# Kernel optimization log

Measured on AMD Instinct MI355X. Metric: run time of the kernel, lower is better.

The kernel has to match this reference:

```python
import jax, jax.numpy as jnp
import numpy as np

NUM_QUERIES = 900
EMBED_DIM = 256
NUM_HEADS = 8
EPS = 1e-5


def bilinear_sample(feats, grid):
    """F.grid_sample(..., align_corners=False, padding_mode='zeros', bilinear).
    feats: [BN, C, H, W], grid: [BN, Q, 2] in [-1,1] (x, y). Returns [BN, Q, C]."""
    BN, C, H, W = feats.shape
    ix = (grid[..., 0] + 1.0) * (W * 0.5) - 0.5
    iy = (grid[..., 1] + 1.0) * (H * 0.5) - 0.5
    x0 = jnp.floor(ix)
    y0 = jnp.floor(iy)
    wx1 = ix - x0
    wy1 = iy - y0
    x0i = x0.astype(jnp.int32)
    y0i = y0.astype(jnp.int32)
    x1i = x0i + 1
    y1i = y0i + 1
    b = jnp.arange(BN)[:, None]

    def gather(yy, xx):
        inb = (xx >= 0) & (xx < W) & (yy >= 0) & (yy < H)
        yc = jnp.clip(yy, 0, H - 1)
        xc = jnp.clip(xx, 0, W - 1)
        v = feats[b, :, yc, xc]  # [BN, Q, C]
        return v * inb[..., None].astype(feats.dtype)

    out = (gather(y0i, x0i) * ((1 - wx1) * (1 - wy1))[..., None]
           + gather(y0i, x1i) * (wx1 * (1 - wy1))[..., None]
           + gather(y1i, x0i) * ((1 - wx1) * wy1)[..., None]
           + gather(y1i, x1i) * (wx1 * wy1)[..., None])
    return out


def setup_inputs() -> dict:
    key = jax.random.key(0)
    ks = jax.random.split(key, 16)
    B, N, C, H, W = 2, 6, 256, 116, 200
    Q, D = NUM_QUERIES, EMBED_DIM
    s = 0.02
    return {
        "image_features": jax.random.normal(ks[0], (B, N, C, H, W), jnp.float32),
        "lidar2img": jax.random.normal(ks[1], (B, N, 4, 4), jnp.float32),
        "query_embedding": jax.random.normal(ks[2], (Q, D), jnp.float32) * s,
        "ref_w": jax.random.normal(ks[3], (3, D), jnp.float32) * s,
        "ref_b": jnp.zeros((3,), jnp.float32),
        "in_proj_w": jax.random.normal(ks[4], (3 * D, D), jnp.float32) * s,
        "in_proj_b": jnp.zeros((3 * D,), jnp.float32),
        "out_proj_w": jax.random.normal(ks[5], (D, D), jnp.float32) * s,
        "out_proj_b": jnp.zeros((D,), jnp.float32),
        "norm_w": jnp.ones((D,), jnp.float32),
        "norm_b": jnp.zeros((D,), jnp.float32),
        "cls_w": jax.random.normal(ks[6], (2, D), jnp.float32) * s,
        "cls_b": jnp.zeros((2,), jnp.float32),
        "box_w": jax.random.normal(ks[7], (6, D), jnp.float32) * s,
        "box_b": jnp.zeros((6,), jnp.float32),
    }


def reference(image_features, lidar2img, query_embedding, ref_w, ref_b,
              in_proj_w, in_proj_b, out_proj_w, out_proj_b,
              norm_w, norm_b, cls_w, cls_b, box_w, box_b):
    B, N, C, H, W = image_features.shape
    Q, D = query_embedding.shape

    q = jnp.broadcast_to(query_embedding[None], (B, Q, D))

    # reference points in [0,1]^3
    ref = jax.nn.sigmoid(q @ ref_w.T + ref_b)  # [B,Q,3]

    # 3D -> 2D projection per camera
    homo = jnp.concatenate([ref, jnp.ones_like(ref[..., :1])], axis=-1)  # [B,Q,4]
    p2h = jnp.einsum('bnij,bqj->bnqi', lidar2img, homo)  # [B,N,Q,4]
    z = p2h[..., 2:3]
    pts2d = p2h[..., 0:2] / (jnp.abs(z) + 1e-5)  # [B,N,Q,2]
    mask = (z > 1e-5)[..., 0]  # [B,N,Q]

    # normalize to [-1,1]
    pn = jnp.stack([pts2d[..., 0] / (W - 1) * 2 - 1,
                    pts2d[..., 1] / (H - 1) * 2 - 1], axis=-1)  # [B,N,Q,2]

    feats_flat = image_features.reshape(B * N, C, H, W)
    grid = pn.reshape(B * N, Q, 2)
    sampled = bilinear_sample(feats_flat, grid)            # [BN,Q,C]
    sampled = sampled.reshape(B, N, Q, C).transpose(0, 2, 1, 3)  # [B,Q,N,C]

    mask_t = mask.transpose(0, 2, 1)[..., None]  # [B,Q,N,1]
    # faithful to torch .view(B,Q,N,2): a raw row-major reshape, not a transpose
    pn_view = pn.reshape(B, Q, N, 2)
    valid = mask_t & (jnp.max(jnp.abs(pn_view), axis=-1, keepdims=True) < 1)  # [B,Q,N,1]
    validf = valid.astype(sampled.dtype)

    sum_feats = jnp.sum(sampled * validf, axis=2)  # [B,Q,C]
    count = jnp.clip(jnp.sum(validf, axis=2), 1.0, None)
    tgt = sum_feats / count

    x = q + tgt  # [B,Q,D]

    # MultiheadAttention (batch_first, 8 heads, no dropout)
    qkv = x @ in_proj_w.T + in_proj_b
    qh, kh, vh = jnp.split(qkv, 3, axis=-1)
    hd = D // NUM_HEADS
    def heads(t):
        return t.reshape(B, Q, NUM_HEADS, hd).transpose(0, 2, 1, 3)  # [B,h,Q,hd]
    qh, kh, vh = heads(qh), heads(kh), heads(vh)
    scores = jnp.einsum('bhqd,bhkd->bhqk', qh, kh) / jnp.sqrt(jnp.asarray(hd, x.dtype))
    attn = jax.nn.softmax(scores, axis=-1)
    o = jnp.einsum('bhqk,bhkd->bhqd', attn, vh).transpose(0, 2, 1, 3).reshape(B, Q, D)
    o = o @ out_proj_w.T + out_proj_b

    # LayerNorm (no residual, faithful to the module)
    mu = jnp.mean(o, axis=-1, keepdims=True)
    var = jnp.mean((o - mu) ** 2, axis=-1, keepdims=True)
    xn = (o - mu) / jnp.sqrt(var + EPS) * norm_w + norm_b

    box = xn @ box_w.T + box_b
    box = jnp.concatenate([jax.nn.sigmoid(box[..., :3]), box[..., 3:]], axis=-1)
    cls = xn @ cls_w.T + cls_b
    return cls, box
```

## Files before the change

kernel.cpp:

```cpp
#include <hip/hip_runtime.h>
#include <math.h>

#define BB 2
#define NCAM 6
#define CC 256
#define HH 116
#define WW 200
#define QQ 900
#define DD 256
#define NHD 8
#define HD 32
#define HWSZ (HH*WW)

__device__ __forceinline__ float sigmoidf_(float x){ return 1.0f/(1.0f+expf(-x)); }

__global__ void proj_kernel(const float* __restrict__ l2i, const float* __restrict__ qe,
        const float* __restrict__ ref_w, const float* __restrict__ ref_b,
        float* __restrict__ wxa, float* __restrict__ wya,
        int* __restrict__ x0a, int* __restrict__ y0a,
        int* __restrict__ maskz, int* __restrict__ inimg) {
    int idx = blockIdx.x*256+threadIdx.x;
    if (idx >= BB*NCAM*QQ) return;
    int q = idx % QQ;
    int bn = idx / QQ;
    float a0 = ref_b[0], a1 = ref_b[1], a2 = ref_b[2];
    const float4* qr = (const float4*)(qe + (size_t)q*DD);
    const float4* w0 = (const float4*)(ref_w);
    const float4* w1 = (const float4*)(ref_w + DD);
    const float4* w2 = (const float4*)(ref_w + 2*DD);
    #pragma unroll 4
    for (int k=0;k<DD/4;k++) {
        float4 a = qr[k];
        float4 b0 = w0[k], b1 = w1[k], b2 = w2[k];
        a0 += a.x*b0.x + a.y*b0.y + a.z*b0.z + a.w*b0.w;
        a1 += a.x*b1.x + a.y*b1.y + a.z*b1.z + a.w*b1.w;
        a2 += a.x*b2.x + a.y*b2.y + a.z*b2.z + a.w*b2.w;
    }
    float h0 = sigmoidf_(a0), h1 = sigmoidf_(a1), h2 = sigmoidf_(a2);
    const float* m = l2i + bn*16;
    float px = m[0]*h0+m[1]*h1+m[2]*h2+m[3];
    float py = m[4]*h0+m[5]*h1+m[6]*h2+m[7];
    float pz = m[8]*h0+m[9]*h1+m[10]*h2+m[11];
    float denom = fabsf(pz)+1e-5f;
    float sx = px/denom, sy = py/denom;
    float pnx = sx/(float)(WW-1)*2.0f-1.0f;
    float pny = sy/(float)(HH-1)*2.0f-1.0f;
    maskz[idx] = (pz > 1e-5f) ? 1 : 0;
    inimg[idx] = (fmaxf(fabsf(pnx),fabsf(pny)) < 1.0f) ? 1 : 0;
    float ix = (pnx+1.0f)*(WW*0.5f)-0.5f;
    float iy = (pny+1.0f)*(HH*0.5f)-0.5f;
    float x0f = floorf(ix), y0f = floorf(iy);
    wxa[idx] = ix-x0f; wya[idx] = iy-y0f;
    x0a[idx] = (int)x0f; y0a[idx] = (int)y0f;
}

__global__ __launch_bounds__(256) void sample_kernel(const float* __restrict__ feats,
        const float* __restrict__ qe, const float* __restrict__ wxa, const float* __restrict__ wya,
        const int* __restrict__ x0a, const int* __restrict__ y0a,
        const int* __restrict__ maskz, const int* __restrict__ inimg,
        float* __restrict__ xout) {
    __shared__ float swx[NCAM], swy[NCAM];
    __shared__ int sx0[NCAM], sy0[NCAM], sval[NCAM];
    int bq = blockIdx.x;
    int b = bq / QQ, q = bq % QQ;
    int t = threadIdx.x;
    if (t < NCAM) {
        int n = t;
        int s = (b*NCAM+n)*QQ + q;
        int sq = b*(NCAM*QQ) + q*NCAM + n;
        sval[n] = maskz[s] & inimg[sq];
        swx[n] = wxa[s]; swy[n] = wya[s];
        sx0[n] = x0a[s]; sy0[n] = y0a[s];
    }
    __syncthreads();
    int c = t;
    float v00[NCAM] = {}, v10[NCAM] = {}, v01[NCAM] = {}, v11[NCAM] = {};
    float W00[NCAM], W10[NCAM], W01[NCAM], W11[NCAM];
    int cnt = 0;
    #pragma unroll
    for (int n = 0; n < NCAM; n++) {
        int valid = sval[n];
        float wx = swx[n], wy = swy[n];
        int x0 = sx0[n], y0 = sy0[n];
        int x1 = x0 + 1, y1 = y0 + 1;
        bool x0in = (unsigned)x0 < (unsigned)WW;
        bool x1in = (unsigned)x1 < (unsigned)WW;
        bool y0in = (unsigned)y0 < (unsigned)HH;
        bool y1in = (unsigned)y1 < (unsigned)HH;
        int x0c = x0in ? x0 : 0;
        int x1c = x1in ? x1 : (WW-1);
        int y0c = y0in ? y0 : 0;
        int y1c = y1in ? y1 : (HH-1);
        W00[n] = (x0in && y0in) ? (1.f-wx)*(1.f-wy) : 0.f;
        W10[n] = (x1in && y0in) ? wx*(1.f-wy) : 0.f;
        W01[n] = (x0in && y1in) ? (1.f-wx)*wy : 0.f;
        W11[n] = (x1in && y1in) ? wx*wy : 0.f;
        cnt += valid;
        if (valid) {
            const float* fb = feats + ((size_t)(b*NCAM+n)*CC + c)*HWSZ;
            const float* r0 = fb + y0c*WW;
            const float* r1 = fb + y1c*WW;
            v00[n] = r0[x0c]; v10[n] = r0[x1c];
            v01[n] = r1[x0c]; v11[n] = r1[x1c];
        }
    }
    float sum = 0.0f;
    #pragma unroll
    for (int n = 0; n < NCAM; n++)
        sum += W00[n]*v00[n] + W10[n]*v10[n] + W01[n]*v01[n] + W11[n]*v11[n];
    float tgt = sum / (float)(cnt > 0 ? cnt : 1);
    xout[(size_t)bq*DD + c] = qe[q*DD+c] + tgt;
}

#define TILE 64
#define BKK 16
template<bool COMB>
__global__ __launch_bounds__(256) void sgemm_nt(const float* __restrict__ A,
        const float* __restrict__ A2, const float* __restrict__ lA, const float* __restrict__ lB,
        const float* __restrict__ Bw, const float* __restrict__ bias,
        float* __restrict__ Cm, int M, int N, int K) {
    __shared__ float As[BKK][TILE+4];
    __shared__ float Bs[BKK][TILE+4];
    int tid = threadIdx.x;
    int m0 = blockIdx.y * TILE, n0 = blockIdx.x * TILE;
    float acc[4][4] = {};
    int tx = tid & 15, ty = tid >> 4;
    int ms = tid >> 2;
    int kq = (tid & 3) * 4;
    for (int k0 = 0; k0 < K; k0 += BKK) {
        int gm = m0 + ms;
        float4 fa = make_float4(0.f,0.f,0.f,0.f);
        if (gm < M) {
            if (COMB) {
                int k = k0 + kq;
                int h = k >> 5, d = k & 31;
                int b = (gm >= QQ) ? 1 : 0;
                int qq_ = gm - b*QQ;
                size_t base = ((size_t)(b*NHD+h))*QQ + qq_;
                const float4 o1 = *(const float4*)(A  + base*HD + d);
                const float4 o2 = *(const float4*)(A2 + base*HD + d);
                float L = lA[base] + lB[base];
                float r = 1.0f / L;
                fa = make_float4((o1.x+o2.x)*r, (o1.y+o2.y)*r, (o1.z+o2.z)*r, (o1.w+o2.w)*r);
            } else {
                fa = *(const float4*)(A + (size_t)gm * K + k0 + kq);
            }
        }
        As[kq+0][ms]=fa.x; As[kq+1][ms]=fa.y; As[kq+2][ms]=fa.z; As[kq+3][ms]=fa.w;
        int gn = n0 + ms;
        float4 fb = (gn < N) ? *(const float4*)(Bw + (size_t)gn * K + k0 + kq)
                             : make_float4(0.f,0.f,0.f,0.f);
        Bs[kq+0][ms]=fb.x; Bs[kq+1][ms]=fb.y; Bs[kq+2][ms]=fb.z; Bs[kq+3][ms]=fb.w;
        __syncthreads();
        #pragma unroll
        for (int k = 0; k < BKK; k++) {
            float a[4], bb[4];
            #pragma unroll
            for (int i = 0; i < 4; i++) a[i] = As[k][ty*4+i];
            #pragma unroll
            for (int j = 0; j < 4; j++) bb[j] = Bs[k][tx*4+j];
            #pragma unroll
            for (int i = 0; i < 4; i++)
                #pragma unroll
                for (int j = 0; j < 4; j++)
                    acc[i][j] += a[i] * bb[j];
        }
        __syncthreads();
    }
    for (int i = 0; i < 4; i++) {
        int gm = m0 + ty*4 + i;
        if (gm >= M) continue;
        for (int j = 0; j < 4; j++) {
            int gn = n0 + tx*4 + j;
            if (gn < N) Cm[(size_t)gm * N + gn] = acc[i][j] + bias[gn];
        }
    }
}

#define QTILE 32
#define KTILE 64
#define NQB 29
__global__ __launch_bounds__(256) void attn_flash(const float* __restrict__ qkv,
        float* __restrict__ opA, float* __restrict__ opB,
        float* __restrict__ lpA, float* __restrict__ lpB) {
    __shared__ __align__(16) float Ks[32][68];
    __shared__ __align__(16) float Vs[64][36];
    __shared__ __align__(16) float Ps[32][68];
    int blk = blockIdx.x;
    int qb = blk % NQB;
    int h  = (blk / NQB) % NHD;
    int b  = (blk / (NQB*NHD)) % BB;
    int ks = blk / (NQB*NHD*BB);
    int q0 = qb * QTILE;
    int tid = threadIdx.x;
    int tx = tid & 15, ty = tid >> 4;

    {
        int q = tid >> 3;
        int dseg = (tid & 7) * 4;
        int gq = q0 + q; if (gq > QQ-1) gq = QQ-1;
        const float4 f = *(const float4*)(qkv + ((size_t)(b*QQ+gq))*768 + h*HD + dseg);
        Ps[dseg+0][q] = f.x; Ps[dseg+1][q] = f.y; Ps[dseg+2][q] = f.z; Ps[dseg+3][q] = f.w;
    }
    __syncthreads();
    float q0r[32], q1r[32];
    #pragma unroll
    for (int d = 0; d < 32; d++) { q0r[d] = Ps[d][ty*2]; q1r[d] = Ps[d][ty*2+1]; }
    __syncthreads();

    float O[2][2] = {};
    float l[2] = {0.f, 0.f};
    const float scale = 0.17677669529663689f;
    int kt0 = ks ? 8 : 0;
    int kt1 = ks ? 15 : 8;

    for (int kt = kt0; kt < kt1; kt++) {
        int k0 = kt * KTILE;
        {
            int k = tid >> 2;
            int dseg = (tid & 3) * 8;
            int gk = k0 + k; if (gk > QQ-1) gk = QQ-1;
            const float* kp = qkv + ((size_t)(b*QQ+gk))*768 + 256 + h*HD + dseg;
            float4 f0 = *(const float4*)(kp);
            float4 f1 = *(const float4*)(kp+4);
            Ks[dseg+0][k]=f0.x; Ks[dseg+1][k]=f0.y; Ks[dseg+2][k]=f0.z; Ks[dseg+3][k]=f0.w;
            Ks[dseg+4][k]=f1.x; Ks[dseg+5][k]=f1.y; Ks[dseg+6][k]=f1.z; Ks[dseg+7][k]=f1.w;
            const float* vp = qkv + ((size_t)(b*QQ+gk))*768 + 512 + h*HD + dseg;
            *(float4*)(&Vs[k][dseg])   = *(const float4*)(vp);
            *(float4*)(&Vs[k][dseg+4]) = *(const float4*)(vp+4);
        }
        __syncthreads();

        float acc[2][4] = {};
        #pragma unroll
        for (int d = 0; d < 32; d++) {
            float4 bk = *(const float4*)(&Ks[d][tx*4]);
            float a0 = q0r[d], a1 = q1r[d];
            acc[0][0] += a0*bk.x; acc[0][1] += a0*bk.y; acc[0][2] += a0*bk.z; acc[0][3] += a0*bk.w;
            acc[1][0] += a1*bk.x; acc[1][1] += a1*bk.y; acc[1][2] += a1*bk.z; acc[1][3] += a1*bk.w;
        }
        #pragma unroll
        for (int i = 0; i < 2; i++) {
            float e[4];
            float rs = 0.f;
            #pragma unroll
            for (int j = 0; j < 4; j++) {
                int gk = k0 + tx*4 + j;
                float v = (gk < QQ) ? __expf(acc[i][j]*scale) : 0.f;
                e[j] = v; rs += v;
            }
            #pragma unroll
            for (int m = 1; m < 16; m <<= 1) rs += __shfl_xor(rs, m, 16);
            l[i] += rs;
            *(float4*)(&Ps[ty*2+i][tx*4]) = make_float4(e[0],e[1],e[2],e[3]);
        }
        __syncthreads();

        #pragma unroll
        for (int k4 = 0; k4 < 16; k4++) {
            float4 p0 = *(const float4*)(&Ps[ty*2][k4*4]);
            float4 p1 = *(const float4*)(&Ps[ty*2+1][k4*4]);
            float2 v0 = *(const float2*)(&Vs[k4*4+0][tx*2]);
            float2 v1 = *(const float2*)(&Vs[k4*4+1][tx*2]);
            float2 v2 = *(const float2*)(&Vs[k4*4+2][tx*2]);
            float2 v3 = *(const float2*)(&Vs[k4*4+3][tx*2]);
            O[0][0] += p0.x*v0.x + p0.y*v1.x + p0.z*v2.x + p0.w*v3.x;
            O[0][1] += p0.x*v0.y + p0.y*v1.y + p0.z*v2.y + p0.w*v3.y;
            O[1][0] += p1.x*v0.x + p1.y*v1.x + p1.z*v2.x + p1.w*v3.x;
            O[1][1] += p1.x*v0.y + p1.y*v1.y + p1.z*v2.y + p1.w*v3.y;
        }
        __syncthreads();
    }

    float* op = ks ? opB : opA;
    float* lp = ks ? lpB : lpA;
    #pragma unroll
    for (int i = 0; i < 2; i++) {
        int gq = q0 + ty*2 + i;
        if (gq < QQ) {
            float* o = op + (((size_t)(b*NHD+h))*QQ + gq)*HD + tx*2;
            o[0] = O[i][0];
            o[1] = O[i][1];
            if (tx == 0) lp[(b*NHD+h)*QQ + gq] = l[i];
        }
    }
}

__global__ __launch_bounds__(256) void final_kernel(const float* __restrict__ o,
    const float* __restrict__ norm_w, const float* __restrict__ norm_b,
    const float* __restrict__ cls_w, const float* __restrict__ cls_b,
    const float* __restrict__ box_w, const float* __restrict__ box_b,
    float* __restrict__ out) {
    __shared__ float s_xn[DD];
    __shared__ float red[8];
    int bq = blockIdx.x;
    int t = threadIdx.x;
    float val = o[(size_t)bq*DD + t];
    float v1 = val, v2 = val*val;
    for (int off=32; off>0; off>>=1) { v1 += __shfl_down(v1, off); v2 += __shfl_down(v2, off); }
    if ((t & 63) == 0) { red[t>>6] = v1; red[4 + (t>>6)] = v2; }
    __syncthreads();
    float ssum = red[0]+red[1]+red[2]+red[3];
    float ssq  = red[4]+red[5]+red[6]+red[7];
    float mu = ssum / (float)DD;
    float var = ssq / (float)DD - mu*mu;
    float inv = 1.0f / sqrtf(var + 1e-5f);
    s_xn[t] = (val - mu)*inv*norm_w[t] + norm_b[t];
    __syncthreads();
    int j = t >> 5, lane = t & 31;
    const float* wrow = (j < 2) ? (cls_w + j*DD) : (box_w + (j-2)*DD);
    float acc = 0.f;
    for (int k=lane; k<DD; k+=32) acc += s_xn[k]*wrow[k];
    for (int off=16; off>0; off>>=1) acc += __shfl_down(acc, off, 32);
    if (lane == 0) {
        if (j < 2) {
            out[(size_t)bq*2 + j] = acc + cls_b[j];
        } else {
            int jj = j-2;
            float v = acc + box_b[jj];
            if (jj < 3) v = sigmoidf_(v);
            out[BB*QQ*2 + (size_t)bq*6 + jj] = v;
        }
    }
}

extern "C" void kernel_launch(void* const* d_in, const int* in_sizes, int n_in,
                              void* d_out, int out_size, void* d_ws, size_t ws_size,
                              hipStream_t stream) {
    const float* feats = (const float*)d_in[0];
    const float* l2i   = (const float*)d_in[1];
    const float* qe    = (const float*)d_in[2];
    const float* ref_w = (const float*)d_in[3];
    const float* ref_b = (const float*)d_in[4];
    const float* ipw   = (const float*)d_in[5];
    const float* ipb   = (const float*)d_in[6];
    const float* opw   = (const float*)d_in[7];
    const float* opb   = (const float*)d_in[8];
    const float* nw    = (const float*)d_in[9];
    const float* nb    = (const float*)d_in[10];
    const float* clsw  = (const float*)d_in[11];
    const float* clsb  = (const float*)d_in[12];
    const float* boxw  = (const float*)d_in[13];
    const float* boxb  = (const float*)d_in[14];
    float* out = (float*)d_out;
    float* ws = (float*)d_ws;

    float* ref   = ws;
    float* wxa   = ws + 2700;
    float* wya   = wxa + 10800;
    int*   x0a   = (int*)(wya + 10800);
    int*   y0a   = x0a + 10800;
    int*   maskz = y0a + 10800;
    int*   inimg = maskz + 10800;
    float* x     = (float*)(inimg + 10800);
    float* qkv   = x + 460800;
    float* attn  = qkv + 1382400;
    float* oproj = attn + 460800;
    (void)ref;

    float* opA = x;
    float* opB = attn;
    float* lpA = wxa;
    float* lpB = wxa + 14400;

    proj_kernel<<<(BB*NCAM*QQ+255)/256, 256, 0, stream>>>(l2i, qe, ref_w, ref_b,
                                                          wxa, wya, x0a, y0a, maskz, inimg);
    sample_kernel<<<BB*QQ, 256, 0, stream>>>(feats, qe, wxa, wya, x0a, y0a, maskz, inimg, x);
    sgemm_nt<false><<<dim3(768/TILE, (BB*QQ+TILE-1)/TILE), 256, 0, stream>>>(
        x, nullptr, nullptr, nullptr, ipw, ipb, qkv, BB*QQ, 768, 256);
    attn_flash<<<BB*NHD*NQB*2, 256, 0, stream>>>(qkv, opA, opB, lpA, lpB);
    sgemm_nt<true><<<dim3(256/TILE, (BB*QQ+TILE-1)/TILE), 256, 0, stream>>>(
        opA, opB, lpA, lpB, opw, opb, oproj, BB*QQ, 256, 256);
    final_kernel<<<BB*QQ, 256, 0, stream>>>(oproj, nw, nb, clsw, clsb, boxw, boxb, out);
}
```

Baseline: 466.1 us.

## Fuse out-projection GEMM, LayerNorm and heads into one tail kernel

Replaces the combining out-projection GEMM and the separate LayerNorm/head kernel with one tail kernel. Each block handles 8 rows: it merges the two attention partials, multiplies by the out-projection weights, then applies LayerNorm and the cls/box heads in shared memory. This removes one launch and the round trip of the projected activations through global memory. In exchange, every block reloads the full 256x256 weight matrix, and each block has fewer rows to reuse it across.

```diff
diff --git a/kernel.cpp b/kernel.cpp
--- a/kernel.cpp
+++ b/kernel.cpp
@@ -114,9 +114,7 @@
 
 #define TILE 64
 #define BKK 16
-template<bool COMB>
 __global__ __launch_bounds__(256) void sgemm_nt(const float* __restrict__ A,
-        const float* __restrict__ A2, const float* __restrict__ lA, const float* __restrict__ lB,
         const float* __restrict__ Bw, const float* __restrict__ bias,
         float* __restrict__ Cm, int M, int N, int K) {
     __shared__ float As[BKK][TILE+4];
@@ -129,23 +127,8 @@
     int kq = (tid & 3) * 4;
     for (int k0 = 0; k0 < K; k0 += BKK) {
         int gm = m0 + ms;
-        float4 fa = make_float4(0.f,0.f,0.f,0.f);
-        if (gm < M) {
-            if (COMB) {
-                int k = k0 + kq;
-                int h = k >> 5, d = k & 31;
-                int b = (gm >= QQ) ? 1 : 0;
-                int qq_ = gm - b*QQ;
-                size_t base = ((size_t)(b*NHD+h))*QQ + qq_;
-                const float4 o1 = *(const float4*)(A  + base*HD + d);
-                const float4 o2 = *(const float4*)(A2 + base*HD + d);
-                float L = lA[base] + lB[base];
-                float r = 1.0f / L;
-                fa = make_float4((o1.x+o2.x)*r, (o1.y+o2.y)*r, (o1.z+o2.z)*r, (o1.w+o2.w)*r);
-            } else {
-                fa = *(const float4*)(A + (size_t)gm * K + k0 + kq);
-            }
-        }
+        float4 fa = (gm < M) ? *(const float4*)(A + (size_t)gm * K + k0 + kq)
+                             : make_float4(0.f,0.f,0.f,0.f);
         As[kq+0][ms]=fa.x; As[kq+1][ms]=fa.y; As[kq+2][ms]=fa.z; As[kq+3][ms]=fa.w;
         int gn = n0 + ms;
         float4 fb = (gn < N) ? *(const float4*)(Bw + (size_t)gn * K + k0 + kq)
@@ -286,40 +269,107 @@
     }
 }
 
-__global__ __launch_bounds__(256) void final_kernel(const float* __restrict__ o,
+#define TM 8
+__global__ __launch_bounds__(256) void tail_kernel(
+    const float* __restrict__ opA, const float* __restrict__ opB,
+    const float* __restrict__ lpA, const float* __restrict__ lpB,
+    const float* __restrict__ opw, const float* __restrict__ opb,
     const float* __restrict__ norm_w, const float* __restrict__ norm_b,
     const float* __restrict__ cls_w, const float* __restrict__ cls_b,
     const float* __restrict__ box_w, const float* __restrict__ box_b,
     float* __restrict__ out) {
-    __shared__ float s_xn[DD];
-    __shared__ float red[8];
-    int bq = blockIdx.x;
+    __shared__ __align__(16) float As[TM][264];
+    __shared__ __align__(16) float Bs[BKK][260];
     int t = threadIdx.x;
-    float val = o[(size_t)bq*DD + t];
-    float v1 = val, v2 = val*val;
-    for (int off=32; off>0; off>>=1) { v1 += __shfl_down(v1, off); v2 += __shfl_down(v2, off); }
-    if ((t & 63) == 0) { red[t>>6] = v1; red[4 + (t>>6)] = v2; }
+    int m0 = blockIdx.x * TM;
+
+    {
+        int r = t >> 5, seg = t & 31;
+        int gm = m0 + r;
+        int b = (gm >= QQ) ? 1 : 0;
+        int qq_ = gm - b*QQ;
+        int h = seg >> 2, d = (seg & 3) * 8;
+        size_t base = ((size_t)(b*NHD+h))*QQ + qq_;
+        float4 a0 = *(const float4*)(opA + base*HD + d);
+        float4 a1 = *(const float4*)(opA + base*HD + d + 4);
+        float4 b0 = *(const float4*)(opB + base*HD + d);
+        float4 b1 = *(const float4*)(opB + base*HD + d + 4);
+        float rcpL = 1.0f / (lpA[base] + lpB[base]);
+        int k = seg * 8;
+        *(float4*)(&As[r][k])   = make_float4((a0.x+b0.x)*rcpL,(a0.y+b0.y)*rcpL,(a0.z+b0.z)*rcpL,(a0.w+b0.w)*rcpL);
+        *(float4*)(&As[r][k+4]) = make_float4((a1.x+b1.x)*rcpL,(a1.y+b1.y)*rcpL,(a1.z+b1.z)*rcpL,(a1.w+b1.w)*rcpL);
+    }
+
+    float acc[TM] = {};
+    int nn = t >> 2, sg = t & 3;
+    for (int k0 = 0; k0 < DD; k0 += BKK) {
+        #pragma unroll
+        for (int ii = 0; ii < 4; ii++) {
+            int n = nn + ii*64;
+            float4 f = *(const float4*)(opw + (size_t)n*DD + k0 + sg*4);
+            Bs[sg*4+0][n]=f.x; Bs[sg*4+1][n]=f.y; Bs[sg*4+2][n]=f.z; Bs[sg*4+3][n]=f.w;
+        }
+        __syncthreads();
+        #pragma unroll
+        for (int kk = 0; kk < 4; kk++) {
+            float b0 = Bs[kk*4+0][t], b1 = Bs[kk*4+1][t], b2 = Bs[kk*4+2][t], b3 = Bs[kk*4+3][t];
+            #pragma unroll
+            for (int r = 0; r < TM; r++) {
+                float4 a = *(const float4*)(&As[r][k0 + kk*4]);
+                acc[r] += a.x*b0 + a.y*b1 + a.z*b2 + a.w*b3;
+            }
+        }
+        __syncthreads();
+    }
+
+    float bn_ = opb[t];
+    #pragma unroll
+    for (int r = 0; r < TM; r++) As[r][t] = acc[r] + bn_;
     __syncthreads();
-    float ssum = red[0]+red[1]+red[2]+red[3];
-    float ssq  = red[4]+red[5]+red[6]+red[7];
-    float mu = ssum / (float)DD;
-    float var = ssq / (float)DD - mu*mu;
-    float inv = 1.0f / sqrtf(var + 1e-5f);
-    s_xn[t] = (val - mu)*inv*norm_w[t] + norm_b[t];
-    __syncthreads();
-    int j = t >> 5, lane = t & 31;
-    const float* wrow = (j < 2) ? (cls_w + j*DD) : (box_w + (j-2)*DD);
-    float acc = 0.f;
-    for (int k=lane; k<DD; k+=32) acc += s_xn[k]*wrow[k];
-    for (int off=16; off>0; off>>=1) acc += __shfl_down(acc, off, 32);
-    if (lane == 0) {
-        if (j < 2) {
-            out[(size_t)bq*2 + j] = acc + cls_b[j];
-        } else {
-            int jj = j-2;
-            float v = acc + box_b[jj];
-            if (jj < 3) v = sigmoidf_(v);
-            out[BB*QQ*2 + (size_t)bq*6 + jj] = v;
+
+    {
+        int r = t >> 5, lane = t & 31;
+        int gm = m0 + r;
+        float s1 = 0.f, s2 = 0.f;
+        #pragma unroll
+        for (int i = 0; i < 8; i++) {
+            float v = As[r][lane + i*32];
+            s1 += v; s2 += v*v;
+        }
+        #pragma unroll
+        for (int off = 16; off > 0; off >>= 1) {
+            s1 += __shfl_down(s1, off, 32);
+            s2 += __shfl_down(s2, off, 32);
+        }
+        s1 = __shfl(s1, 0, 32);
+        s2 = __shfl(s2, 0, 32);
+        float mu = s1 / (float)DD;
+        float var = s2 / (float)DD - mu*mu;
+        float inv = 1.0f / sqrtf(var + 1e-5f);
+        #pragma unroll
+        for (int i = 0; i < 8; i++) {
+            int k = lane + i*32;
+            As[r][k] = (As[r][k] - mu)*inv*norm_w[k] + norm_b[k];
+        }
+        int j = lane >> 2, kb = lane & 3;
+        const float* wrow = (j < 2) ? (cls_w + j*DD) : (box_w + (j-2)*DD);
+        float accd = 0.f;
+        #pragma unroll 16
+        for (int i = 0; i < 64; i++) {
+            int k = kb + i*4;
+            accd += As[r][k] * wrow[k];
+        }
+        accd += __shfl_xor(accd, 1, 4);
+        accd += __shfl_xor(accd, 2, 4);
+        if (kb == 0) {
+            if (j < 2) {
+                out[(size_t)gm*2 + j] = accd + cls_b[j];
+            } else {
+                int jj = j - 2;
+                float v = accd + box_b[jj];
+                if (jj < 3) v = sigmoidf_(v);
+                out[BB*QQ*2 + (size_t)gm*6 + jj] = v;
+            }
         }
     }
 }
@@ -345,7 +395,6 @@
     float* out = (float*)d_out;
     float* ws = (float*)d_ws;
 
-    float* ref   = ws;
     float* wxa   = ws + 2700;
     float* wya   = wxa + 10800;
     int*   x0a   = (int*)(wya + 10800);
@@ -355,8 +404,6 @@
     float* x     = (float*)(inimg + 10800);
     float* qkv   = x + 460800;
     float* attn  = qkv + 1382400;
-    float* oproj = attn + 460800;
-    (void)ref;
 
     float* opA = x;
     float* opB = attn;
@@ -366,10 +413,9 @@
     proj_kernel<<<(BB*NCAM*QQ+255)/256, 256, 0, stream>>>(l2i, qe, ref_w, ref_b,
                                                           wxa, wya, x0a, y0a, maskz, inimg);
     sample_kernel<<<BB*QQ, 256, 0, stream>>>(feats, qe, wxa, wya, x0a, y0a, maskz, inimg, x);
-    sgemm_nt<false><<<dim3(768/TILE, (BB*QQ+TILE-1)/TILE), 256, 0, stream>>>(
-        x, nullptr, nullptr, nullptr, ipw, ipb, qkv, BB*QQ, 768, 256);
+    sgemm_nt<<<dim3(768/TILE, (BB*QQ+TILE-1)/TILE), 256, 0, stream>>>(
+        x, ipw, ipb, qkv, BB*QQ, 768, 256);
     attn_flash<<<BB*NHD*NQB*2, 256, 0, stream>>>(qkv, opA, opB, lpA, lpB);
-    sgemm_nt<true><<<dim3(256/TILE, (BB*QQ+TILE-1)/TILE), 256, 0, stream>>>(
-        opA, opB, lpA, lpB, opw, opb, oproj, BB*QQ, 256, 256);
-    final_kernel<<<BB*QQ, 256, 0, stream>>>(oproj, nw, nb, clsw, clsb, boxw, boxb, out);
-}
+    tail_kernel<<<(BB*QQ)/TM, 256, 0, stream>>>(opA, opB, lpA, lpB, opw, opb,
+                                                nw, nb, clsw, clsb, boxw, boxb, out);
+}
```

After: 462.0 us. Within noise of the previous version (-0.9%).
